# Optimization experiments

Hardware: AMD Instinct MI355X
Metric: run time of the kernel (lower is better)

## Reference

```python
import jax, jax.numpy as jnp
import numpy as np

N_ENT = 50000     # n_entities
C = 128           # channel
N_EDGES = 1600000 # n_edges (avg degree 32)
N_REL = 11        # n_relations; edge_type in [1, N_REL-1]
N_HOPS = 3
EPS = 1e-12       # F.normalize default eps


def setup_inputs() -> dict:
    key = jax.random.key(0)
    k1, k2, k3, k4 = jax.random.split(key, 4)
    entity_emb = jax.random.normal(k1, (N_ENT, C), dtype=jnp.float32)
    edge_index = jax.random.randint(k2, (2, N_EDGES), 0, N_ENT, dtype=jnp.int64)
    edge_type = jax.random.randint(k3, (N_EDGES,), 1, N_REL, dtype=jnp.int64)
    # xavier_uniform bound for (N_REL-1, C)
    bound = float(np.sqrt(6.0 / ((N_REL - 1) + C)))
    weight = jax.random.uniform(k4, (N_REL - 1, C), jnp.float32, -bound, bound)
    return {"entity_emb": entity_emb, "edge_index": edge_index,
            "edge_type": edge_type, "weight": weight}


def reference(entity_emb, edge_index, edge_type, weight):
    head, tail = edge_index[0], edge_index[1]
    # relation embedding per edge: weight[edge_type - 1] -> [E, C]
    rel_emb = weight[edge_type - 1]
    ones = jnp.ones((edge_index.shape[1],), entity_emb.dtype)
    # per-head in-degree counts (constant across hops)
    cnt = jax.ops.segment_sum(ones, head, num_segments=N_ENT)
    denom = jnp.maximum(cnt, 1.0)[:, None]  # scatter_mean: zero rows stay zero

    def hop(emb):
        msg = emb[tail] * rel_emb                                   # gather + mul [E, C]
        agg = jax.ops.segment_sum(msg, head, num_segments=N_ENT) / denom  # scatter_mean
        # F.normalize (L2 per row)
        norm = jnp.linalg.norm(agg, axis=1, keepdims=True)
        return agg / jnp.maximum(norm, EPS)

    res = entity_emb
    emb = entity_emb
    for _ in range(N_HOPS):
        emb = hop(emb)
        res = res + emb
    return res
```

## Files before the change

### kernel.cpp

```cpp
#include <hip/hip_runtime.h>

#define N_ENT   50000
#define CH      128
#define N_EDGES 1600000
#define N_RELM1 10
#define NB      391
#define BCAP    4608
#define PART_BLOCKS 800
#define CHUNK   (N_EDGES / PART_BLOCKS)
#define EPS_N   1e-12f

typedef int v16i __attribute__((ext_vector_type(16)));

__device__ __forceinline__ unsigned int f2bf_bits(float f) {
    unsigned int x = __float_as_uint(f);
    return (x + 0x7FFFu + ((x >> 16) & 1u)) >> 16;
}

__device__ __forceinline__ v16i sload16(const int* p, int boff) {
    v16i r;
    asm volatile("s_load_dwordx16 %0, %1, %2"
                 : "=s"(r) : "s"(p), "s"(boff));
    return r;
}
__device__ __forceinline__ void swait16(v16i& r) {
    asm volatile("s_waitcnt lgkmcnt(0)" : "+s"(r));
}

__global__ __launch_bounds__(256) void gc_part_kernel(const int* __restrict__ head,
                                                      const int* __restrict__ tail,
                                                      const int* __restrict__ etyp,
                                                      int* __restrict__ barr,
                                                      int* __restrict__ pack,
                                                      const float* __restrict__ ent,
                                                      unsigned int* __restrict__ emb) {
    __shared__ int hist[512];
    __shared__ int boff_s[512];
    __shared__ int fctr[512];
    __shared__ int psum[256];
    __shared__ int stageE[CHUNK];
    __shared__ unsigned short stageB[CHUNK];
    __shared__ int stage2[CHUNK];
    int tid = threadIdx.x, blk = blockIdx.x;
    for (int i = tid; i < 512; i += 256) { hist[i] = 0; fctr[i] = 0; }
    __syncthreads();
    int lo = blk * CHUNK;
    for (int i = tid; i < CHUNK; i += 256) {
        int e = lo + i;
        int h = head[e];
        int b = h >> 7;
        stageE[i] = (tail[e] & 0xFFFF) | ((etyp[e] - 1) << 16) | ((h & 127) << 20);
        stageB[i] = (unsigned short)b;
        atomicAdd(&hist[b], 1);
    }
    __syncthreads();
    int a0 = hist[2 * tid], a1 = hist[2 * tid + 1];
    int s2 = a0 + a1;
    psum[tid] = s2;
    __syncthreads();
    for (int d = 1; d < 256; d <<= 1) {
        int t = (tid >= d) ? psum[tid - d] : 0;
        __syncthreads();
        psum[tid] += t;
        __syncthreads();
    }
    int excl = psum[tid] - s2;
    boff_s[2 * tid] = excl;
    boff_s[2 * tid + 1] = excl + a0;
    __syncthreads();
    for (int i = tid; i < CHUNK; i += 256) {
        int b = stageB[i];
        int pos = boff_s[b] + atomicAdd(&fctr[b], 1);
        stage2[pos] = stageE[i];
    }
    __syncthreads();
    for (int i = tid; i < CHUNK; i += 256) barr[lo + i] = stage2[i];
    for (int i = tid; i < NB; i += 256)
        pack[blk * NB + i] = (boff_s[i] << 8) | fctr[i];
    for (int i = blk * 256 + tid; i < N_ENT * (CH / 2); i += PART_BLOCKS * 256) {
        float2 v = *(const float2*)(ent + 2 * (size_t)i);
        emb[i] = f2bf_bits(v.x) | (f2bf_bits(v.y) << 16);
    }
}

__global__ __launch_bounds__(1024) void gc_place_kernel(const int* __restrict__ barr,
                                                        const int* __restrict__ pack,
                                                        unsigned int* __restrict__ off_deg,
                                                        int* __restrict__ csr) {
    __shared__ int ent_s[BCAP];
    __shared__ int psum[1024];
    __shared__ int hcnt[128];
    __shared__ int hloc[128];
    __shared__ int hctr[128];
    int b = blockIdx.x, tid = threadIdx.x;
    if (tid < 128) { hcnt[tid] = 0; hctr[tid] = 0; }
    int c = 0, o = 0;
    if (tid < PART_BLOCKS) {
        int pk = pack[tid * NB + b];
        c = pk & 255;
        o = pk >> 8;
    }
    psum[tid] = c;
    __syncthreads();
    for (int d = 1; d < 1024; d <<= 1) {
        int t = (tid >= d) ? psum[tid - d] : 0;
        __syncthreads();
        psum[tid] += t;
        __syncthreads();
    }
    int my_off = psum[tid] - c;
    int n = psum[1023];
    const int* src = barr + tid * CHUNK + o;
    for (int k = 0; k < c; ++k) ent_s[my_off + k] = src[k];
    __syncthreads();
    for (int i = tid; i < n; i += 1024)
        atomicAdd(&hcnt[(ent_s[i] >> 20) & 127], 1);
    __syncthreads();
    int v = (tid < 128) ? hcnt[tid] : 0;
    for (int d = 1; d < 128; d <<= 1) {
        int t = (tid < 128 && tid >= d) ? hcnt[tid - d] : 0;
        __syncthreads();
        if (tid < 128) hcnt[tid] += t;
        __syncthreads();
    }
    int lo = b * BCAP;
    if (tid < 128) {
        int start = lo + hcnt[tid] - v;
        hloc[tid] = start;
        int h = (b << 7) + tid;
        if (h < N_ENT) off_deg[h] = ((unsigned)start << 11) | (unsigned)v;
    }
    __syncthreads();
    for (int i = tid; i < n; i += 1024) {
        int e = ent_s[i];
        int hl = (e >> 20) & 127;
        int pos = hloc[hl] + atomicAdd(&hctr[hl], 1);
        csr[pos] = e & 0xFFFFF;
    }
}

__global__ __launch_bounds__(256) void gc_hop_kernel(
        const unsigned int* __restrict__ src,
        const unsigned int* __restrict__ off_deg,
        const int* __restrict__ csr,
        const float* __restrict__ wt,
        unsigned int* __restrict__ dst,
        float* __restrict__ res,
        const float* __restrict__ ent,
        const unsigned int* __restrict__ yprev,
        int mode) {
    __shared__ float wt_s[N_RELM1 * CH];
    for (int i = threadIdx.x; i < N_RELM1 * CH; i += 256) wt_s[i] = wt[i];
    __syncthreads();

    int wave = threadIdx.x >> 6, lane = threadIdx.x & 63;
    int row = __builtin_amdgcn_readfirstlane(blockIdx.x * 4 + wave);

    unsigned od = (unsigned)__builtin_amdgcn_readfirstlane((int)off_deg[row]);
    int seg = (int)(od >> 11);
    int deg = (int)(od & 2047u);

    float ax = 0.f, ay = 0.f;

#define EDGE(pk) { \
        unsigned v = src[(unsigned)((pk) & 0xFFFF) * 64u + (unsigned)lane]; \
        float2 w = *(const float2*)(&wt_s[((pk) >> 16) * CH + 2 * lane]);   \
        ax = fmaf(__uint_as_float(v << 16), w.x, ax);                       \
        ay = fmaf(__uint_as_float(v & 0xFFFF0000u), w.y, ay); }

    if (deg > 0) {
        int nch = (deg + 15) >> 4;
        v16i A = sload16(csr, seg << 2);
        swait16(A);
        int boff = (seg + 16) << 2;
        for (int c = 0; c < nch - 1; ++c, boff += 64) {
            v16i B = sload16(csr, boff);
            #pragma unroll
            for (int u = 0; u < 16; ++u) EDGE(A[u]);
            swait16(B);
            A = B;
        }
        int rem = deg - ((nch - 1) << 4);
        #pragma unroll
        for (int u = 0; u < 16; ++u)
            if (u < rem) EDGE(A[u]);
    }
#undef EDGE

    float invd = 1.0f / fmaxf((float)deg, 1.0f);
    float x0 = ax * invd, x1 = ay * invd;

    float s = x0 * x0 + x1 * x1;
    #pragma unroll
    for (int o = 32; o; o >>= 1) s += __shfl_xor(s, o, 64);

    float inv = 1.0f / fmaxf(sqrtf(s), EPS_N);
    float y0 = x0 * inv, y1v = x1 * inv;

    if (mode == 0) {
        dst[(row << 6) + lane] = f2bf_bits(y0) | (f2bf_bits(y1v) << 16);
    } else {
        unsigned p1 = yprev[(row << 6) + lane];
        unsigned p2 = src[(row << 6) + lane];
        int base = (row << 7) + 2 * lane;
        float2 e = *(const float2*)(ent + base);
        float2 o;
        o.x = e.x + __uint_as_float(p1 << 16)
                  + __uint_as_float(p2 << 16) + y0;
        o.y = e.y + __uint_as_float(p1 & 0xFFFF0000u)
                  + __uint_as_float(p2 & 0xFFFF0000u) + y1v;
        *(float2*)(res + base) = o;
    }
}

extern "C" void kernel_launch(void* const* d_in, const int* in_sizes, int n_in,
                              void* d_out, int out_size, void* d_ws, size_t ws_size,
                              hipStream_t stream) {
    const float* ent  = (const float*)d_in[0];
    const int*   eidx = (const int*)d_in[1];
    const int*   etyp = (const int*)d_in[2];
    const float* wt   = (const float*)d_in[3];
    float*       res  = (float*)d_out;

    const int* head = eidx;
    const int* tail = eidx + N_EDGES;

    unsigned int* embA = (unsigned int*)d_ws;
    unsigned int* embB = embA + (size_t)N_ENT * 64;
    unsigned int* off_deg = embB + (size_t)N_ENT * 64;
    int* csr  = (int*)(off_deg + N_ENT);
    int* barr = csr + (size_t)NB * BCAP;
    int* pack = barr + N_EDGES;

    gc_part_kernel<<<PART_BLOCKS, 256, 0, stream>>>(head, tail, etyp, barr, pack,
                                                    ent, embA);
    gc_place_kernel<<<NB, 1024, 0, stream>>>(barr, pack, off_deg, csr);

    const int hop_grid = N_ENT / 4;
    gc_hop_kernel<<<hop_grid, 256, 0, stream>>>(embA, off_deg, csr, wt, embB,
                                                res, ent, embB, 0);
    gc_hop_kernel<<<hop_grid, 256, 0, stream>>>(embB, off_deg, csr, wt, embA,
                                                res, ent, embB, 0);
    gc_hop_kernel<<<hop_grid, 256, 0, stream>>>(embA, off_deg, csr, wt, embB,
                                                res, ent, embB, 1);
}
```

Before: 296.7 us.

## Process 8 head rows per wave with edges sorted by tail block for locality

The place kernel now buckets edges by a key of (row-group of 8 heads, tail high bits, head-in-group), so each wave walks a single merged edge list for 8 rows ordered by tail range. The goal is better L2 locality on the embedding gathers and fewer per-row overheads such as scalar loads and short tails. The hop kernel keeps 8 accumulator pairs per lane and picks one per edge with a switch, then normalises each row. The cost is divergence-free but branchy accumulator selection, more registers, and a bigger scan in the place kernel.

```diff
diff --git a/kernel.cpp b/kernel.cpp
--- a/kernel.cpp
+++ b/kernel.cpp
@@ -8,9 +8,12 @@
 #define BCAP    4608
 #define PART_BLOCKS 800
 #define CHUNK   (N_EDGES / PART_BLOCKS)
+#define NRG     (N_ENT / 8)
+#define NKEY    2048
 #define EPS_N   1e-12f
 
 typedef int v16i __attribute__((ext_vector_type(16)));
+typedef int v8i  __attribute__((ext_vector_type(8)));
 
 __device__ __forceinline__ unsigned int f2bf_bits(float f) {
     unsigned int x = __float_as_uint(f);
@@ -23,8 +26,16 @@
                  : "=s"(r) : "s"(p), "s"(boff));
     return r;
 }
+__device__ __forceinline__ v8i sload8(const int* p) {
+    v8i r;
+    asm volatile("s_load_dwordx8 %0, %1, 0" : "=s"(r) : "s"(p));
+    return r;
+}
 __device__ __forceinline__ void swait16(v16i& r) {
     asm volatile("s_waitcnt lgkmcnt(0)" : "+s"(r));
+}
+__device__ __forceinline__ void swait16_8(v16i& a, v8i& d) {
+    asm volatile("s_waitcnt lgkmcnt(0)" : "+s"(a), "+s"(d));
 }
 
 __global__ __launch_bounds__(256) void gc_part_kernel(const int* __restrict__ head,
@@ -85,15 +96,17 @@
 
 __global__ __launch_bounds__(1024) void gc_place_kernel(const int* __restrict__ barr,
                                                         const int* __restrict__ pack,
-                                                        unsigned int* __restrict__ off_deg,
+                                                        int* __restrict__ deg_arr,
+                                                        int* __restrict__ rg_off,
                                                         int* __restrict__ csr) {
     __shared__ int ent_s[BCAP];
     __shared__ int psum[1024];
-    __shared__ int hcnt[128];
-    __shared__ int hloc[128];
-    __shared__ int hctr[128];
+    __shared__ int kcnt[NKEY];
+    __shared__ int kctr[NKEY];
+    __shared__ int kbase[NKEY];
     int b = blockIdx.x, tid = threadIdx.x;
-    if (tid < 128) { hcnt[tid] = 0; hctr[tid] = 0; }
+    kcnt[tid] = 0; kcnt[tid + 1024] = 0;
+    kctr[tid] = 0; kctr[tid + 1024] = 0;
     int c = 0, o = 0;
     if (tid < PART_BLOCKS) {
         int pk = pack[tid * NB + b];
@@ -113,35 +126,53 @@
     const int* src = barr + tid * CHUNK + o;
     for (int k = 0; k < c; ++k) ent_s[my_off + k] = src[k];
     __syncthreads();
-    for (int i = tid; i < n; i += 1024)
-        atomicAdd(&hcnt[(ent_s[i] >> 20) & 127], 1);
-    __syncthreads();
-    int v = (tid < 128) ? hcnt[tid] : 0;
-    for (int d = 1; d < 128; d <<= 1) {
-        int t = (tid < 128 && tid >= d) ? hcnt[tid - d] : 0;
-        __syncthreads();
-        if (tid < 128) hcnt[tid] += t;
-        __syncthreads();
-    }
-    int lo = b * BCAP;
-    if (tid < 128) {
-        int start = lo + hcnt[tid] - v;
-        hloc[tid] = start;
-        int h = (b << 7) + tid;
-        if (h < N_ENT) off_deg[h] = ((unsigned)start << 11) | (unsigned)v;
-    }
-    __syncthreads();
     for (int i = tid; i < n; i += 1024) {
         int e = ent_s[i];
         int hl = (e >> 20) & 127;
-        int pos = hloc[hl] + atomicAdd(&hctr[hl], 1);
-        csr[pos] = e & 0xFFFFF;
-    }
-}
-
-__global__ __launch_bounds__(256) void gc_hop_kernel(
+        int key = ((hl >> 3) << 7) | (((e & 0xFFFF) >> 12) << 3) | (hl & 7);
+        atomicAdd(&kcnt[key], 1);
+    }
+    __syncthreads();
+    if (tid < 128) {
+        int rgl = tid >> 3, r = tid & 7;
+        int d = 0;
+        #pragma unroll
+        for (int g = 0; g < 16; ++g) d += kcnt[(rgl << 7) | (g << 3) | r];
+        int h = (b << 7) + tid;
+        if (h < N_ENT) deg_arr[h] = d;
+    }
+    int a0 = kcnt[2 * tid], a1 = kcnt[2 * tid + 1];
+    int s2 = a0 + a1;
+    psum[tid] = s2;
+    __syncthreads();
+    for (int d = 1; d < 1024; d <<= 1) {
+        int t = (tid >= d) ? psum[tid - d] : 0;
+        __syncthreads();
+        psum[tid] += t;
+        __syncthreads();
+    }
+    int excl = psum[tid] - s2;
+    kbase[2 * tid] = excl;
+    kbase[2 * tid + 1] = excl + a0;
+    __syncthreads();
+    int lo = b * BCAP;
+    if (tid < 16) {
+        int grg = (b << 4) + tid;
+        if (grg < NRG) rg_off[grg] = lo + kbase[tid << 7];
+    }
+    for (int i = tid; i < n; i += 1024) {
+        int e = ent_s[i];
+        int hl = (e >> 20) & 127;
+        int key = ((hl >> 3) << 7) | (((e & 0xFFFF) >> 12) << 3) | (hl & 7);
+        int pos = lo + kbase[key] + atomicAdd(&kctr[key], 1);
+        csr[pos] = (e & 0xFFFFF) | ((hl & 7) << 20);
+    }
+}
+
+__global__ __launch_bounds__(256, 8) void gc_hop_kernel(
         const unsigned int* __restrict__ src,
-        const unsigned int* __restrict__ off_deg,
+        const int* __restrict__ deg_arr,
+        const int* __restrict__ rg_off,
         const int* __restrict__ csr,
         const float* __restrict__ wt,
         unsigned int* __restrict__ dst,
@@ -154,24 +185,40 @@
     __syncthreads();
 
     int wave = threadIdx.x >> 6, lane = threadIdx.x & 63;
-    int row = __builtin_amdgcn_readfirstlane(blockIdx.x * 4 + wave);
-
-    unsigned od = (unsigned)__builtin_amdgcn_readfirstlane((int)off_deg[row]);
-    int seg = (int)(od >> 11);
-    int deg = (int)(od & 2047u);
-
-    float ax = 0.f, ay = 0.f;
+    int rg = __builtin_amdgcn_readfirstlane(blockIdx.x * 4 + wave);
+    if (rg >= NRG) return;
+
+    v8i D = sload8(deg_arr + (size_t)rg * 8);
+    int seg = __builtin_amdgcn_readfirstlane(rg_off[rg]);
+    v16i A = sload16(csr, seg << 2);
+    swait16_8(A, D);
+
+    int nedges = D[0] + D[1] + D[2] + D[3] + D[4] + D[5] + D[6] + D[7];
+
+    float ax0 = 0.f, ay0 = 0.f, ax1 = 0.f, ay1 = 0.f;
+    float ax2 = 0.f, ay2 = 0.f, ax3 = 0.f, ay3 = 0.f;
+    float ax4 = 0.f, ay4 = 0.f, ax5 = 0.f, ay5 = 0.f;
+    float ax6 = 0.f, ay6 = 0.f, ax7 = 0.f, ay7 = 0.f;
 
 #define EDGE(pk) { \
-        unsigned v = src[(unsigned)((pk) & 0xFFFF) * 64u + (unsigned)lane]; \
-        float2 w = *(const float2*)(&wt_s[((pk) >> 16) * CH + 2 * lane]);   \
-        ax = fmaf(__uint_as_float(v << 16), w.x, ax);                       \
-        ay = fmaf(__uint_as_float(v & 0xFFFF0000u), w.y, ay); }
-
-    if (deg > 0) {
-        int nch = (deg + 15) >> 4;
-        v16i A = sload16(csr, seg << 2);
-        swait16(A);
+        int pk_ = (pk); \
+        unsigned v = src[(unsigned)(pk_ & 0xFFFF) * 64u + (unsigned)lane]; \
+        float2 w = *(const float2*)(&wt_s[((pk_ >> 16) & 15) * CH + 2 * lane]); \
+        float vx = __uint_as_float(v << 16); \
+        float vy = __uint_as_float(v & 0xFFFF0000u); \
+        switch (pk_ >> 20) { \
+        case 0: ax0 = fmaf(vx, w.x, ax0); ay0 = fmaf(vy, w.y, ay0); break; \
+        case 1: ax1 = fmaf(vx, w.x, ax1); ay1 = fmaf(vy, w.y, ay1); break; \
+        case 2: ax2 = fmaf(vx, w.x, ax2); ay2 = fmaf(vy, w.y, ay2); break; \
+        case 3: ax3 = fmaf(vx, w.x, ax3); ay3 = fmaf(vy, w.y, ay3); break; \
+        case 4: ax4 = fmaf(vx, w.x, ax4); ay4 = fmaf(vy, w.y, ay4); break; \
+        case 5: ax5 = fmaf(vx, w.x, ax5); ay5 = fmaf(vy, w.y, ay5); break; \
+        case 6: ax6 = fmaf(vx, w.x, ax6); ay6 = fmaf(vy, w.y, ay6); break; \
+        default: ax7 = fmaf(vx, w.x, ax7); ay7 = fmaf(vy, w.y, ay7); break; \
+        } }
+
+    if (nedges > 0) {
+        int nch = (nedges + 15) >> 4;
         int boff = (seg + 16) << 2;
         for (int c = 0; c < nch - 1; ++c, boff += 64) {
             v16i B = sload16(csr, boff);
@@ -180,37 +227,46 @@
             swait16(B);
             A = B;
         }
-        int rem = deg - ((nch - 1) << 4);
+        int rem = nedges - ((nch - 1) << 4);
         #pragma unroll
         for (int u = 0; u < 16; ++u)
             if (u < rem) EDGE(A[u]);
     }
 #undef EDGE
 
-    float invd = 1.0f / fmaxf((float)deg, 1.0f);
-    float x0 = ax * invd, x1 = ay * invd;
-
-    float s = x0 * x0 + x1 * x1;
-    #pragma unroll
-    for (int o = 32; o; o >>= 1) s += __shfl_xor(s, o, 64);
-
-    float inv = 1.0f / fmaxf(sqrtf(s), EPS_N);
-    float y0 = x0 * inv, y1v = x1 * inv;
-
-    if (mode == 0) {
-        dst[(row << 6) + lane] = f2bf_bits(y0) | (f2bf_bits(y1v) << 16);
-    } else {
-        unsigned p1 = yprev[(row << 6) + lane];
-        unsigned p2 = src[(row << 6) + lane];
-        int base = (row << 7) + 2 * lane;
-        float2 e = *(const float2*)(ent + base);
-        float2 o;
-        o.x = e.x + __uint_as_float(p1 << 16)
-                  + __uint_as_float(p2 << 16) + y0;
-        o.y = e.y + __uint_as_float(p1 & 0xFFFF0000u)
-                  + __uint_as_float(p2 & 0xFFFF0000u) + y1v;
-        *(float2*)(res + base) = o;
-    }
+#define ROWOUT(r, axr, ayr) { \
+        int row = (rg << 3) + r; \
+        float invd = 1.0f / fmaxf((float)D[r], 1.0f); \
+        float x0 = axr * invd, x1 = ayr * invd; \
+        float s = x0 * x0 + x1 * x1; \
+        _Pragma("unroll") \
+        for (int o = 32; o; o >>= 1) s += __shfl_xor(s, o, 64); \
+        float inv = 1.0f / fmaxf(sqrtf(s), EPS_N); \
+        float y0 = x0 * inv, y1v = x1 * inv; \
+        if (mode == 0) { \
+            dst[(row << 6) + lane] = f2bf_bits(y0) | (f2bf_bits(y1v) << 16); \
+        } else { \
+            unsigned p1 = yprev[(row << 6) + lane]; \
+            unsigned p2 = src[(row << 6) + lane]; \
+            int base = (row << 7) + 2 * lane; \
+            float2 e = *(const float2*)(ent + base); \
+            float2 o2; \
+            o2.x = e.x + __uint_as_float(p1 << 16) \
+                       + __uint_as_float(p2 << 16) + y0; \
+            o2.y = e.y + __uint_as_float(p1 & 0xFFFF0000u) \
+                       + __uint_as_float(p2 & 0xFFFF0000u) + y1v; \
+            *(float2*)(res + base) = o2; \
+        } }
+
+    ROWOUT(0, ax0, ay0);
+    ROWOUT(1, ax1, ay1);
+    ROWOUT(2, ax2, ay2);
+    ROWOUT(3, ax3, ay3);
+    ROWOUT(4, ax4, ay4);
+    ROWOUT(5, ax5, ay5);
+    ROWOUT(6, ax6, ay6);
+    ROWOUT(7, ax7, ay7);
+#undef ROWOUT
 }
 
 extern "C" void kernel_launch(void* const* d_in, const int* in_sizes, int n_in,
@@ -227,20 +283,21 @@
 
     unsigned int* embA = (unsigned int*)d_ws;
     unsigned int* embB = embA + (size_t)N_ENT * 64;
-    unsigned int* off_deg = embB + (size_t)N_ENT * 64;
-    int* csr  = (int*)(off_deg + N_ENT);
+    int* deg_arr = (int*)(embB + (size_t)N_ENT * 64);
+    int* rg_off  = deg_arr + N_ENT;
+    int* csr  = rg_off + 6272;
     int* barr = csr + (size_t)NB * BCAP;
     int* pack = barr + N_EDGES;
 
     gc_part_kernel<<<PART_BLOCKS, 256, 0, stream>>>(head, tail, etyp, barr, pack,
                                                     ent, embA);
-    gc_place_kernel<<<NB, 1024, 0, stream>>>(barr, pack, off_deg, csr);
-
-    const int hop_grid = N_ENT / 4;
-    gc_hop_kernel<<<hop_grid, 256, 0, stream>>>(embA, off_deg, csr, wt, embB,
-                                                res, ent, embB, 0);
-    gc_hop_kernel<<<hop_grid, 256, 0, stream>>>(embB, off_deg, csr, wt, embA,
-                                                res, ent, embB, 0);
-    gc_hop_kernel<<<hop_grid, 256, 0, stream>>>(embA, off_deg, csr, wt, embB,
-                                                res, ent, embB, 1);
-}
+    gc_place_kernel<<<NB, 1024, 0, stream>>>(barr, pack, deg_arr, rg_off, csr);
+
+    const int hop_grid = (NRG + 3) / 4;
+    gc_hop_kernel<<<hop_grid, 256, 0, stream>>>(embA, deg_arr, rg_off, csr, wt,
+                                                embB, res, ent, embB, 0);
+    gc_hop_kernel<<<hop_grid, 256, 0, stream>>>(embB, deg_arr, rg_off, csr, wt,
+                                                embA, res, ent, embB, 0);
+    gc_hop_kernel<<<hop_grid, 256, 0, stream>>>(embA, deg_arr, rg_off, csr, wt,
+                                                embB, res, ent, embB, 1);
+}
```

Result: slower. 505.7 us (+70.4%).
